# Kernel tuning notes

Measured on AMD Instinct MI355X. Metric: run time of the kernel, lower is better.

Reference implementation:

```python
import jax, jax.numpy as jnp
import numpy as np

BS, QLEN, DIM, NHEADS, SEG = 2, 2048, 640, 8, 5
C = DIM // SEG * (SEG - 1)  # 512, channels kept after aggregator
AGG = DIM // SEG            # 128, aggregated channel slice


def setup_inputs() -> dict:
    key = jax.random.key(0)
    ks = jax.random.split(key, 12)
    s = 0.02
    return {
        "Q": jax.random.normal(ks[0], (BS, QLEN, DIM), jnp.float32),
        # Linear weights stored [in, out] so y = x @ W + b
        "W_Q": jax.random.normal(ks[1], (DIM, DIM), jnp.float32) * s,
        "b_Q": jnp.zeros((DIM,), jnp.float32),
        "W_K": jax.random.normal(ks[2], (DIM, DIM), jnp.float32) * s,
        "b_K": jnp.zeros((DIM,), jnp.float32),
        "W_V": jax.random.normal(ks[3], (DIM, DIM), jnp.float32) * s,
        "b_V": jnp.zeros((DIM,), jnp.float32),
        "W_pos": jax.random.uniform(ks[4], (QLEN, C), jnp.float32, -0.02, 0.02),
        "W_agg": jax.random.normal(ks[5], (AGG, AGG), jnp.float32) * s,
        "b_agg": jnp.zeros((AGG,), jnp.float32),
        "W_out": jax.random.normal(ks[6], (DIM, DIM), jnp.float32) * s,
        "b_out": jnp.zeros((DIM,), jnp.float32),
    }


def reference(Q, W_Q, b_Q, W_K, b_K, W_V, b_V, W_pos, W_agg, b_agg, W_out, b_out):
    bs, L, dim = Q.shape
    hd = C // NHEADS  # per-head dim after aggregation (64)
    # self-attention: K = V = Q
    q = Q @ W_Q + b_Q
    k = Q @ W_K + b_K
    v = Q @ W_V + b_V
    qkv = jnp.stack([q, k, v])  # [3, bs, L, dim]
    # Aggregator: keep first 4/5 channels per branch, aggregate last 1/5 across q/k/v
    x_main = qkv[..., :C]                                   # [3, bs, L, C]
    x_agg0 = jax.nn.gelu(qkv[..., C:].mean(0) @ W_agg + b_agg)  # [bs, L, AGG]
    # pos embedding add (dropout is identity at eval)
    q_s = (x_main[0] + W_pos).reshape(bs, L, NHEADS, hd).transpose(0, 2, 1, 3)  # [bs,H,L,hd]
    k_s = (x_main[1] + W_pos).reshape(bs, L, NHEADS, hd).transpose(0, 2, 3, 1)  # [bs,H,hd,L]
    v_s = (x_main[2] + W_pos).reshape(bs, L, NHEADS, hd).transpose(0, 2, 1, 3)  # [bs,H,L,hd]
    scale = (DIM // NHEADS) ** -0.5  # note: uses dim//n_heads (80), not post-agg head dim
    scores = jnp.einsum("bhqd,bhdk->bhqk", q_s, k_s) * scale  # [bs,H,L,L]
    attn = jax.nn.softmax(scores, axis=-1)
    out = jnp.einsum("bhqk,bhkd->bhqd", attn, v_s)             # [bs,H,L,hd]
    out = out.transpose(0, 2, 1, 3).reshape(bs, L, C)
    out = jnp.concatenate([out, x_agg0], axis=-1) @ W_out + b_out  # [bs,L,dim]
    return out, attn
```

## Files before the change

### kernel.cpp

```cpp
#include <hip/hip_runtime.h>
#include <cstdint>
#include <cstddef>

#define BSZ   2
#define QL    2048
#define DIMN  640
#define NH    8
#define CMAIN 512
#define AGGD  128
#define MROWS 4096
#define SCALE_QK 0.11180339887498948f
#define C2EXP (SCALE_QK * 1.4426950408889634f)

typedef __bf16 bf16;
typedef __bf16 bf16x8 __attribute__((ext_vector_type(8)));
typedef __bf16 bf16x4v __attribute__((ext_vector_type(4)));
typedef float  f32x4  __attribute__((ext_vector_type(4)));

typedef __attribute__((address_space(1))) const uint32_t GU32;
typedef __attribute__((address_space(3))) uint32_t LU32;
#define GLL(g, l) __builtin_amdgcn_global_load_lds((GU32*)(g), (LU32*)(l), 16, 0, 0)

#define EXP2F(x) __builtin_amdgcn_exp2f(x)
#define LOG2F(x) __builtin_amdgcn_logf(x)

static __device__ __forceinline__ f32x4 mfma16(bf16x8 a, bf16x8 b, f32x4 c) {
    return __builtin_amdgcn_mfma_f32_16x16x32_bf16(a, b, c, 0, 0, 0);
}

static __device__ __forceinline__ void waitbar() {
    asm volatile("s_waitcnt vmcnt(0)" ::: "memory");
    __builtin_amdgcn_s_barrier();
    asm volatile("" ::: "memory");
}

template<int ROWB>
static __device__ __forceinline__ bf16x8 ldsfragR(const bf16* base, int row, int kbyte) {
    return *(const bf16x8*)((const char*)base + row * ROWB + (kbyte ^ ((row & 7) << 4)));
}

template<int NCH, int ROWB>
static __device__ __forceinline__ void stage_rowsR(bf16* ldsbuf, const char* gbase,
                                                   int strideB, int tid) {
    const int w = tid >> 6, lane = tid & 63;
    #pragma unroll
    for (int i = 0; i < NCH / 256; ++i) {
        int c = i * 256 + w * 64 + lane;
        int r = c / (ROWB / 16);
        int kb = ((c % (ROWB / 16)) * 16) ^ ((r & 7) << 4);
        GLL(gbase + (size_t)r * strideB + kb,
            (char*)ldsbuf + (size_t)(i * 256 + w * 64) * 16);
    }
}

template<int MI>
static __device__ __forceinline__ void gemm_main(
    const bf16* __restrict__ A, const bf16* __restrict__ BT,
    int m0, int n0, bf16* lds, f32x4 acc[MI][4])
{
    const int tid = threadIdx.x;
    const int w = tid >> 6, lane = tid & 63;
    const int lr = lane & 15, lg = lane >> 4;
    const int wm = (w >> 1) * (MI * 16), wn = (w & 1) * 64;
    constexpr int ASZ = MI * 2048;
    constexpr int BUF = ASZ + 8192;

    stage_rowsR<MI * 256, 128>(lds,   (const char*)(A + (size_t)m0 * 640), 1280, tid);
    stage_rowsR<1024, 128>(lds + ASZ, (const char*)(BT + (size_t)n0 * 640), 1280, tid);
    int cur = 0;
    #pragma unroll 1
    for (int ch = 0; ch < 10; ++ch) {
        waitbar();
        if (ch < 9) {
            int kk = (ch + 1) * 64;
            bf16* nb = lds + (cur ^ 1) * BUF;
            stage_rowsR<MI * 256, 128>(nb,   (const char*)(A + (size_t)m0 * 640 + kk), 1280, tid);
            stage_rowsR<1024, 128>(nb + ASZ, (const char*)(BT + (size_t)n0 * 640 + kk), 1280, tid);
        }
        const bf16* cA = lds + cur * BUF;
        const bf16* cB = cA + ASZ;
        #pragma unroll
        for (int ks = 0; ks < 2; ++ks) {
            bf16x8 a[MI], b[4];
            #pragma unroll
            for (int i = 0; i < MI; ++i) a[i] = ldsfragR<128>(cA, wm + i * 16 + lr, ks * 64 + lg * 16);
            #pragma unroll
            for (int i = 0; i < 4; ++i)  b[i] = ldsfragR<128>(cB, wn + i * 16 + lr, ks * 64 + lg * 16);
            #pragma unroll
            for (int mi = 0; mi < MI; ++mi)
                #pragma unroll
                for (int ni = 0; ni < 4; ++ni)
                    acc[mi][ni] = mfma16(a[mi], b[ni], acc[mi][ni]);
        }
        cur ^= 1;
    }
}

__global__ void __launch_bounds__(256) k_split_q(const float* __restrict__ Q,
                                                 bf16* __restrict__ Qbf) {
    int i = blockIdx.x * 256 + threadIdx.x;
    float4 v = ((const float4*)Q)[i];
    bf16x4v hv;
    hv[0] = (bf16)v.x; hv[1] = (bf16)v.y; hv[2] = (bf16)v.z; hv[3] = (bf16)v.w;
    *(bf16x4v*)(Qbf + (size_t)i * 4) = hv;
}

__global__ void __launch_bounds__(256) k_prep_w(
    const float* __restrict__ WQ, const float* __restrict__ WK,
    const float* __restrict__ WV, const float* __restrict__ WO,
    bf16* __restrict__ BTqkv, bf16* __restrict__ BTout)
{
    __shared__ float tl[64][65];
    const int ty = blockIdx.x / 10, tx = blockIdx.x % 10;
    const int wsel = blockIdx.y;
    const float* W = (wsel == 0) ? WQ : (wsel == 1) ? WK : (wsel == 2) ? WV : WO;
    const int tid = threadIdx.x;
    const int rr = tid >> 4;
    const int cc = (tid & 15) * 4;
    #pragma unroll
    for (int i = 0; i < 4; ++i) {
        int k = tx * 64 + rr + i * 16;
        float4 v = *(const float4*)(W + (size_t)k * 640 + ty * 64 + cc);
        tl[cc + 0][rr + i * 16] = v.x;
        tl[cc + 1][rr + i * 16] = v.y;
        tl[cc + 2][rr + i * 16] = v.z;
        tl[cc + 3][rr + i * 16] = v.w;
    }
    __syncthreads();
    bf16* dst; int nbase;
    if (wsel < 3) { dst = BTqkv; nbase = wsel * 640 + ty * 64; }
    else          { dst = BTout; nbase = ty * 64; }
    const int nl0 = tid >> 4;
    const int kl = (tid & 15) * 4;
    #pragma unroll
    for (int i = 0; i < 4; ++i) {
        int nl = nl0 + i * 16;
        bf16x4v hv;
        #pragma unroll
        for (int j = 0; j < 4; ++j) hv[j] = (bf16)tl[nl][kl + j];
        *(bf16x4v*)(dst + (size_t)(nbase + nl) * 640 + tx * 64 + kl) = hv;
    }
}

__global__ void __launch_bounds__(256) k_gemm_qkv(
    const bf16* __restrict__ Qbf, const bf16* __restrict__ BT,
    const float* __restrict__ bQ, const float* __restrict__ bK, const float* __restrict__ bV,
    const float* __restrict__ Wpos,
    bf16* __restrict__ qsbuf, bf16* __restrict__ vsT, float* __restrict__ aggbuf)
{
    __shared__ __align__(16) bf16 lds[2 * (8192 + 8192)];
    const int m0 = blockIdx.x * 128, n0 = blockIdx.y * 128;
    f32x4 acc[4][4];
    {
        f32x4 z = {0.f, 0.f, 0.f, 0.f};
        #pragma unroll
        for (int mi = 0; mi < 4; ++mi)
            #pragma unroll
            for (int ni = 0; ni < 4; ++ni) acc[mi][ni] = z;
    }
    gemm_main<4>(Qbf, BT, m0, n0, lds, acc);

    const int tid = threadIdx.x, w = tid >> 6, lane = tid & 63;
    const int lr = lane & 15, lg = lane >> 4;
    const int wm = (w >> 1) * 64, wn = (w & 1) * 64;
    const int p = n0 / 640;
    const float* bias = (p == 0) ? bQ : (p == 1) ? bK : bV;

    #pragma unroll
    for (int mi = 0; mi < 4; ++mi)
        #pragma unroll
        for (int ni = 0; ni < 4; ++ni) {
            int n = n0 + wn + ni * 16 + lr;
            int c = n - p * 640;
            int rbase = m0 + wm + mi * 16 + lg * 4;
            float bval = bias[c];
            if (c < 512) {
                int hh = c >> 6, d = c & 63;
                #pragma unroll
                for (int r = 0; r < 4; ++r) {
                    int rg = rbase + r;
                    int bb = rg >> 11, l = rg & 2047;
                    float v = acc[mi][ni][r] + bval + Wpos[(size_t)l * 512 + c];
                    if (p < 2)
                        qsbuf[(((size_t)(p * 2 + bb) * 8 + hh) * 2048 + l) * 64 + d] = (bf16)v;
                    else
                        vsT[(((size_t)(bb * 8 + hh)) * 64 + d) * 2048 + l] = (bf16)v;
                }
            } else {
                int j = c - 512;
                #pragma unroll
                for (int r = 0; r < 4; ++r) {
                    int rg = rbase + r;
                    aggbuf[((size_t)p * MROWS + rg) * AGGD + j] = acc[mi][ni][r] + bval;
                }
            }
        }
}

__global__ void __launch_bounds__(256) k_agg(const float* __restrict__ aggbuf,
                                             const float* __restrict__ Wagg, const float* __restrict__ bagg,
                                             bf16* __restrict__ xcat)
{
    __shared__ float wl[128 * 128];
    __shared__ float xl[32 * 128];
    const int tid = threadIdx.x;
    const int r0 = blockIdx.x * 32;
    for (int i = tid; i < 128 * 128; i += 256) wl[i] = Wagg[i];
    for (int i = tid; i < 32 * 128; i += 256) {
        int row = i >> 7, j = i & 127;
        size_t rg = r0 + row;
        float s = aggbuf[rg * AGGD + j]
                + aggbuf[((size_t)MROWS + rg) * AGGD + j]
                + aggbuf[((size_t)2 * MROWS + rg) * AGGD + j];
        xl[i] = s * (1.0f / 3.0f);
    }
    __syncthreads();
    const int row = tid >> 3;
    const int jo0 = (tid & 7) * 16;
    float acc[16];
    #pragma unroll
    for (int jj = 0; jj < 16; ++jj) acc[jj] = 0.f;
    for (int j = 0; j < 128; ++j) {
        float xv = xl[row * 128 + j];
        const float* wr = &wl[j * 128 + jo0];
        #pragma unroll
        for (int jj = 0; jj < 16; ++jj) acc[jj] = fmaf(xv, wr[jj], acc[jj]);
    }
    size_t rg = r0 + row;
    #pragma unroll
    for (int jj = 0; jj < 16; ++jj) {
        float t = acc[jj] + bagg[jo0 + jj];
        float g = 0.5f * t * (1.0f + tanhf(0.7978845608028654f * (t + 0.044715f * t * t * t)));
        xcat[rg * 640 + 512 + jo0 + jj] = (bf16)g;
    }
}

__global__ void __launch_bounds__(256) k_attn(const bf16* __restrict__ qsbuf, const bf16* __restrict__ vsT,
                                              float* __restrict__ gattn,
                                              bf16* __restrict__ xcat)
{
    __shared__ __align__(16) bf16 smem[2][16384];
    __shared__ __align__(16) bf16 p_lds[4][16 * 128];

    const int bh = blockIdx.y;
    const int b = bh >> 3, h = bh & 7;
    const int q0 = blockIdx.x * 64;
    const int tid = threadIdx.x, w = tid >> 6, lane = tid & 63;
    const int lr = lane & 15, lg = lane >> 4;

    const bf16* qbase = qsbuf + (size_t)(b * 8 + h) * (2048 * 64);
    const bf16* kbase = qsbuf + (size_t)((2 + b) * 8 + h) * (2048 * 64);
    const bf16* vtb   = vsT + (size_t)(b * 8 + h) * (64 * 2048);

    bf16x8 aq[2];
    {
        const bf16* qp = qbase + (size_t)(q0 + w * 16 + lr) * 64 + lg * 8;
        aq[0] = *(const bf16x8*)(qp);
        aq[1] = *(const bf16x8*)(qp + 32);
    }

    float lsum = 0.f;
    stage_rowsR<1024, 128>(smem[0], (const char*)kbase, 128, tid);
    int cur = 0;
    #pragma unroll 1
    for (int kt = 0; kt < 16; ++kt) {
        waitbar();
        if (kt < 15)
            stage_rowsR<1024, 128>(smem[cur ^ 1], (const char*)kbase + (size_t)(kt + 1) * 16384, 128, tid);
        __builtin_amdgcn_sched_barrier(0);
        const bf16* kb = smem[cur];
        f32x4 s[8];
        {
            f32x4 z = {0.f, 0.f, 0.f, 0.f};
            #pragma unroll
            for (int ni = 0; ni < 8; ++ni) s[ni] = z;
        }
        #pragma unroll
        for (int ks = 0; ks < 2; ++ks)
            #pragma unroll
            for (int ni = 0; ni < 8; ++ni)
                s[ni] = mfma16(ldsfragR<128>(kb, ni * 16 + lr, ks * 64 + lg * 16), aq[ks], s[ni]);
        #pragma unroll
        for (int ni = 0; ni < 8; ++ni)
            #pragma unroll
            for (int r = 0; r < 4; ++r)
                lsum += EXP2F(s[ni][r] * C2EXP);
        cur ^= 1;
    }
    lsum += __shfl_xor(lsum, 16);
    lsum += __shfl_xor(lsum, 32);
    const float l2i = -LOG2F(lsum);

    f32x4 o[4];
    {
        f32x4 z = {0.f, 0.f, 0.f, 0.f};
        #pragma unroll
        for (int ni = 0; ni < 4; ++ni) o[ni] = z;
    }
    float* attnrow = gattn + (size_t)bh * 2048 * 2048 + (size_t)(q0 + w * 16 + lr) * 2048;

    stage_rowsR<1024, 128>(smem[0],        (const char*)kbase, 128, tid);
    stage_rowsR<1024, 256>(smem[0] + 8192, (const char*)vtb, 4096, tid);
    cur = 0;
    #pragma unroll 1
    for (int kt = 0; kt < 16; ++kt) {
        if (kt == 0) asm volatile("s_waitcnt vmcnt(0)" ::: "memory");
        else         asm volatile("s_waitcnt vmcnt(8)" ::: "memory");
        __builtin_amdgcn_s_barrier();
        asm volatile("" ::: "memory");
        if (kt < 15) {
            stage_rowsR<1024, 128>(smem[cur ^ 1],        (const char*)kbase + (size_t)(kt + 1) * 16384, 128, tid);
            stage_rowsR<1024, 256>(smem[cur ^ 1] + 8192, (const char*)vtb + (size_t)(kt + 1) * 256, 4096, tid);
        }
        __builtin_amdgcn_sched_barrier(0);
        const bf16* kb = smem[cur];
        const bf16* vb = smem[cur] + 8192;
        f32x4 s[8];
        {
            f32x4 z = {0.f, 0.f, 0.f, 0.f};
            #pragma unroll
            for (int ni = 0; ni < 8; ++ni) s[ni] = z;
        }
        #pragma unroll
        for (int ks = 0; ks < 2; ++ks)
            #pragma unroll
            for (int ni = 0; ni < 8; ++ni)
                s[ni] = mfma16(ldsfragR<128>(kb, ni * 16 + lr, ks * 64 + lg * 16), aq[ks], s[ni]);
        bf16* pl = &p_lds[w][0];
        float* arow = attnrow + kt * 128;
        #pragma unroll
        for (int ni = 0; ni < 8; ++ni) {
            f32x4 p;
            #pragma unroll
            for (int r = 0; r < 4; ++r) p[r] = EXP2F(fmaf(s[ni][r], C2EXP, l2i));
            *(f32x4*)(arow + ni * 16 + lg * 4) = p;
            bf16x4v pb;
            #pragma unroll
            for (int r = 0; r < 4; ++r) pb[r] = (bf16)p[r];
            *(bf16x4v*)((char*)pl + lr * 256 + ((ni * 32 + lg * 8) ^ ((lr & 7) << 4))) = pb;
        }
        #pragma unroll
        for (int ks = 0; ks < 4; ++ks) {
            bf16x8 pa = ldsfragR<256>(pl, lr, ks * 64 + lg * 16);
            #pragma unroll
            for (int ni = 0; ni < 4; ++ni)
                o[ni] = mfma16(pa, ldsfragR<256>(vb, ni * 16 + lr, ks * 64 + lg * 16), o[ni]);
        }
        cur ^= 1;
    }

    #pragma unroll
    for (int ni = 0; ni < 4; ++ni) {
        #pragma unroll
        for (int r = 0; r < 4; ++r) {
            int qr = q0 + w * 16 + lg * 4 + r;
            size_t rg = (size_t)b * 2048 + qr;
            int c = h * 64 + ni * 16 + lr;
            xcat[rg * 640 + c] = (bf16)o[ni][r];
        }
    }
}

__global__ void __launch_bounds__(256) k_gemm_out(
    const bf16* __restrict__ X, const bf16* __restrict__ BT,
    const float* __restrict__ bout, float* __restrict__ out0)
{
    __shared__ __align__(16) bf16 lds[2 * (4096 + 8192)];
    const int m0 = blockIdx.x * 64, n0 = blockIdx.y * 128;
    f32x4 acc[2][4];
    {
        f32x4 z = {0.f, 0.f, 0.f, 0.f};
        #pragma unroll
        for (int mi = 0; mi < 2; ++mi)
            #pragma unroll
            for (int ni = 0; ni < 4; ++ni) acc[mi][ni] = z;
    }
    gemm_main<2>(X, BT, m0, n0, lds, acc);

    const int tid = threadIdx.x, w = tid >> 6, lane = tid & 63;
    const int lr = lane & 15, lg = lane >> 4;
    const int wm = (w >> 1) * 32, wn = (w & 1) * 64;
    #pragma unroll
    for (int mi = 0; mi < 2; ++mi)
        #pragma unroll
        for (int ni = 0; ni < 4; ++ni) {
            int n = n0 + wn + ni * 16 + lr;
            float bv = bout[n];
            #pragma unroll
            for (int r = 0; r < 4; ++r) {
                int rg = m0 + wm + mi * 16 + lg * 4 + r;
                out0[(size_t)rg * 640 + n] = acc[mi][ni][r] + bv;
            }
        }
}

extern "C" void kernel_launch(void* const* d_in, const int* in_sizes, int n_in,
                              void* d_out, int out_size, void* d_ws, size_t ws_size,
                              hipStream_t stream)
{
    (void)in_sizes; (void)n_in; (void)out_size; (void)ws_size;
    const float* Q    = (const float*)d_in[0];
    const float* WQ   = (const float*)d_in[1];
    const float* bQ   = (const float*)d_in[2];
    const float* WK   = (const float*)d_in[3];
    const float* bK   = (const float*)d_in[4];
    const float* WV   = (const float*)d_in[5];
    const float* bV   = (const float*)d_in[6];
    const float* Wpos = (const float*)d_in[7];
    const float* Wagg = (const float*)d_in[8];
    const float* bagg = (const float*)d_in[9];
    const float* WO   = (const float*)d_in[10];
    const float* bout = (const float*)d_in[11];

    float* out0  = (float*)d_out;
    float* gattn = out0 + (size_t)MROWS * DIMN;

    char* ws = (char*)d_ws;
    bf16* Qbf    = (bf16*)(ws);                 ws += (size_t)MROWS * DIMN * 2;
    bf16* BTqkv  = (bf16*)(ws);                 ws += (size_t)1920 * 640 * 2;
    bf16* BTout  = (bf16*)(ws);                 ws += (size_t)640 * 640 * 2;
    bf16* qsbuf  = (bf16*)(ws);                 ws += (size_t)4 * 8 * 2048 * 64 * 2;
    bf16* vsT    = (bf16*)(ws);                 ws += (size_t)16 * 64 * 2048 * 2;
    float* aggbuf= (float*)(ws);                ws += (size_t)3 * MROWS * AGGD * 4;
    bf16* xcat   = (bf16*)(ws);                 ws += (size_t)MROWS * DIMN * 2;

    k_split_q<<<dim3(2560), dim3(256), 0, stream>>>(Q, Qbf);
    k_prep_w<<<dim3(100, 4), dim3(256), 0, stream>>>(WQ, WK, WV, WO, BTqkv, BTout);
    k_gemm_qkv<<<dim3(32, 15), dim3(256), 0, stream>>>(Qbf, BTqkv,
                                                       bQ, bK, bV, Wpos, qsbuf, vsT, aggbuf);
    k_agg<<<dim3(128), dim3(256), 0, stream>>>(aggbuf, Wagg, bagg, xcat);
    k_attn<<<dim3(32, 16), dim3(256), 0, stream>>>(qsbuf, vsT, gattn, xcat);
    k_gemm_out<<<dim3(64, 5), dim3(256), 0, stream>>>(xcat, BTout, bout, out0);
}
```

Baseline: 157.9 us.

## Shrink attention blocks to two waves with 64-key tiles, swizzled grid, fused prep

The attention kernel moves from 256-thread blocks over 64 query rows to 128-thread blocks over 32 query rows. Its second pass now walks 64-key tiles instead of 128-key tiles, with smaller LDS buffers, and a flat grid that is swizzled across heads. The aim is more resident blocks per CU and better spread of the memory-bound attention-probability writes. The Q conversion and weight-transpose kernels are merged into one launch to save launch overhead. The cost is twice the barrier and staging iterations per key sweep, and the K tiles in the first pass are re-read by more blocks.

```diff
diff --git a/kernel.cpp b/kernel.cpp
--- a/kernel.cpp
+++ b/kernel.cpp
@@ -39,17 +39,18 @@
     return *(const bf16x8*)((const char*)base + row * ROWB + (kbyte ^ ((row & 7) << 4)));
 }
 
-template<int NCH, int ROWB>
+template<int NCH, int ROWB, int NT>
 static __device__ __forceinline__ void stage_rowsR(bf16* ldsbuf, const char* gbase,
                                                    int strideB, int tid) {
-    const int w = tid >> 6, lane = tid & 63;
-    #pragma unroll
-    for (int i = 0; i < NCH / 256; ++i) {
-        int c = i * 256 + w * 64 + lane;
+    const int lane = tid & 63;
+    const int wbase = tid - lane;
+    #pragma unroll
+    for (int i = 0; i < NCH / NT; ++i) {
+        int c = i * NT + tid;
         int r = c / (ROWB / 16);
         int kb = ((c % (ROWB / 16)) * 16) ^ ((r & 7) << 4);
         GLL(gbase + (size_t)r * strideB + kb,
-            (char*)ldsbuf + (size_t)(i * 256 + w * 64) * 16);
+            (char*)ldsbuf + (size_t)(i * NT + wbase) * 16);
     }
 }
 
@@ -65,8 +66,8 @@
     constexpr int ASZ = MI * 2048;
     constexpr int BUF = ASZ + 8192;
 
-    stage_rowsR<MI * 256, 128>(lds,   (const char*)(A + (size_t)m0 * 640), 1280, tid);
-    stage_rowsR<1024, 128>(lds + ASZ, (const char*)(BT + (size_t)n0 * 640), 1280, tid);
+    stage_rowsR<MI * 256, 128, 256>(lds,   (const char*)(A + (size_t)m0 * 640), 1280, tid);
+    stage_rowsR<1024, 128, 256>(lds + ASZ, (const char*)(BT + (size_t)n0 * 640), 1280, tid);
     int cur = 0;
     #pragma unroll 1
     for (int ch = 0; ch < 10; ++ch) {
@@ -74,8 +75,8 @@
         if (ch < 9) {
             int kk = (ch + 1) * 64;
             bf16* nb = lds + (cur ^ 1) * BUF;
-            stage_rowsR<MI * 256, 128>(nb,   (const char*)(A + (size_t)m0 * 640 + kk), 1280, tid);
-            stage_rowsR<1024, 128>(nb + ASZ, (const char*)(BT + (size_t)n0 * 640 + kk), 1280, tid);
+            stage_rowsR<MI * 256, 128, 256>(nb,   (const char*)(A + (size_t)m0 * 640 + kk), 1280, tid);
+            stage_rowsR<1024, 128, 256>(nb + ASZ, (const char*)(BT + (size_t)n0 * 640 + kk), 1280, tid);
         }
         const bf16* cA = lds + cur * BUF;
         const bf16* cB = cA + ASZ;
@@ -96,25 +97,27 @@
     }
 }
 
-__global__ void __launch_bounds__(256) k_split_q(const float* __restrict__ Q,
-                                                 bf16* __restrict__ Qbf) {
-    int i = blockIdx.x * 256 + threadIdx.x;
-    float4 v = ((const float4*)Q)[i];
-    bf16x4v hv;
-    hv[0] = (bf16)v.x; hv[1] = (bf16)v.y; hv[2] = (bf16)v.z; hv[3] = (bf16)v.w;
-    *(bf16x4v*)(Qbf + (size_t)i * 4) = hv;
-}
-
-__global__ void __launch_bounds__(256) k_prep_w(
-    const float* __restrict__ WQ, const float* __restrict__ WK,
-    const float* __restrict__ WV, const float* __restrict__ WO,
-    bf16* __restrict__ BTqkv, bf16* __restrict__ BTout)
+__global__ void __launch_bounds__(256) k_prep(
+    const float* __restrict__ Q, const float* __restrict__ WQ,
+    const float* __restrict__ WK, const float* __restrict__ WV,
+    const float* __restrict__ WO,
+    bf16* __restrict__ Qbf, bf16* __restrict__ BTqkv, bf16* __restrict__ BTout)
 {
     __shared__ float tl[64][65];
-    const int ty = blockIdx.x / 10, tx = blockIdx.x % 10;
-    const int wsel = blockIdx.y;
+    const int tid = threadIdx.x;
+    if (blockIdx.x < 2560) {
+        int i = blockIdx.x * 256 + tid;
+        float4 v = ((const float4*)Q)[i];
+        bf16x4v hv;
+        hv[0] = (bf16)v.x; hv[1] = (bf16)v.y; hv[2] = (bf16)v.z; hv[3] = (bf16)v.w;
+        *(bf16x4v*)(Qbf + (size_t)i * 4) = hv;
+        return;
+    }
+    const int f = blockIdx.x - 2560;
+    const int wsel = f / 100;
+    const int rem = f - wsel * 100;
+    const int ty = rem / 10, tx = rem - (rem / 10) * 10;
     const float* W = (wsel == 0) ? WQ : (wsel == 1) ? WK : (wsel == 2) ? WV : WO;
-    const int tid = threadIdx.x;
     const int rr = tid >> 4;
     const int cc = (tid & 15) * 4;
     #pragma unroll
@@ -235,16 +238,18 @@
     }
 }
 
-__global__ void __launch_bounds__(256) k_attn(const bf16* __restrict__ qsbuf, const bf16* __restrict__ vsT,
+__global__ void __launch_bounds__(128) k_attn(const bf16* __restrict__ qsbuf, const bf16* __restrict__ vsT,
                                               float* __restrict__ gattn,
                                               bf16* __restrict__ xcat)
 {
-    __shared__ __align__(16) bf16 smem[2][16384];
-    __shared__ __align__(16) bf16 p_lds[4][16 * 128];
-
-    const int bh = blockIdx.y;
+    __shared__ __align__(16) bf16 smem[2][8192];
+    __shared__ __align__(16) bf16 p_lds[2][1024];
+
+    const int flat = blockIdx.x;
+    const int swz = (flat & 7) * 128 + (flat >> 3);
+    const int bh = swz >> 6;
+    const int q0 = (swz & 63) * 32;
     const int b = bh >> 3, h = bh & 7;
-    const int q0 = blockIdx.x * 64;
     const int tid = threadIdx.x, w = tid >> 6, lane = tid & 63;
     const int lr = lane & 15, lg = lane >> 4;
 
@@ -260,13 +265,13 @@
     }
 
     float lsum = 0.f;
-    stage_rowsR<1024, 128>(smem[0], (const char*)kbase, 128, tid);
+    stage_rowsR<1024, 128, 128>(smem[0], (const char*)kbase, 128, tid);
     int cur = 0;
     #pragma unroll 1
     for (int kt = 0; kt < 16; ++kt) {
         waitbar();
         if (kt < 15)
-            stage_rowsR<1024, 128>(smem[cur ^ 1], (const char*)kbase + (size_t)(kt + 1) * 16384, 128, tid);
+            stage_rowsR<1024, 128, 128>(smem[cur ^ 1], (const char*)kbase + (size_t)(kt + 1) * 16384, 128, tid);
         __builtin_amdgcn_sched_barrier(0);
         const bf16* kb = smem[cur];
         f32x4 s[8];
@@ -299,37 +304,37 @@
     }
     float* attnrow = gattn + (size_t)bh * 2048 * 2048 + (size_t)(q0 + w * 16 + lr) * 2048;
 
-    stage_rowsR<1024, 128>(smem[0],        (const char*)kbase, 128, tid);
-    stage_rowsR<1024, 256>(smem[0] + 8192, (const char*)vtb, 4096, tid);
+    stage_rowsR<512, 128, 128>(smem[0],        (const char*)kbase, 128, tid);
+    stage_rowsR<512, 128, 128>(smem[0] + 4096, (const char*)vtb, 4096, tid);
     cur = 0;
     #pragma unroll 1
-    for (int kt = 0; kt < 16; ++kt) {
+    for (int kt = 0; kt < 32; ++kt) {
         if (kt == 0) asm volatile("s_waitcnt vmcnt(0)" ::: "memory");
-        else         asm volatile("s_waitcnt vmcnt(8)" ::: "memory");
+        else         asm volatile("s_waitcnt vmcnt(4)" ::: "memory");
         __builtin_amdgcn_s_barrier();
         asm volatile("" ::: "memory");
-        if (kt < 15) {
-            stage_rowsR<1024, 128>(smem[cur ^ 1],        (const char*)kbase + (size_t)(kt + 1) * 16384, 128, tid);
-            stage_rowsR<1024, 256>(smem[cur ^ 1] + 8192, (const char*)vtb + (size_t)(kt + 1) * 256, 4096, tid);
+        if (kt < 31) {
+            stage_rowsR<512, 128, 128>(smem[cur ^ 1],        (const char*)kbase + (size_t)(kt + 1) * 8192, 128, tid);
+            stage_rowsR<512, 128, 128>(smem[cur ^ 1] + 4096, (const char*)vtb + (size_t)(kt + 1) * 128, 4096, tid);
         }
         __builtin_amdgcn_sched_barrier(0);
         const bf16* kb = smem[cur];
-        const bf16* vb = smem[cur] + 8192;
-        f32x4 s[8];
+        const bf16* vb = smem[cur] + 4096;
+        f32x4 s[4];
         {
             f32x4 z = {0.f, 0.f, 0.f, 0.f};
             #pragma unroll
-            for (int ni = 0; ni < 8; ++ni) s[ni] = z;
+            for (int ni = 0; ni < 4; ++ni) s[ni] = z;
         }
         #pragma unroll
         for (int ks = 0; ks < 2; ++ks)
             #pragma unroll
-            for (int ni = 0; ni < 8; ++ni)
+            for (int ni = 0; ni < 4; ++ni)
                 s[ni] = mfma16(ldsfragR<128>(kb, ni * 16 + lr, ks * 64 + lg * 16), aq[ks], s[ni]);
         bf16* pl = &p_lds[w][0];
-        float* arow = attnrow + kt * 128;
-        #pragma unroll
-        for (int ni = 0; ni < 8; ++ni) {
+        float* arow = attnrow + kt * 64;
+        #pragma unroll
+        for (int ni = 0; ni < 4; ++ni) {
             f32x4 p;
             #pragma unroll
             for (int r = 0; r < 4; ++r) p[r] = EXP2F(fmaf(s[ni][r], C2EXP, l2i));
@@ -337,14 +342,14 @@
             bf16x4v pb;
             #pragma unroll
             for (int r = 0; r < 4; ++r) pb[r] = (bf16)p[r];
-            *(bf16x4v*)((char*)pl + lr * 256 + ((ni * 32 + lg * 8) ^ ((lr & 7) << 4))) = pb;
-        }
-        #pragma unroll
-        for (int ks = 0; ks < 4; ++ks) {
-            bf16x8 pa = ldsfragR<256>(pl, lr, ks * 64 + lg * 16);
+            *(bf16x4v*)((char*)pl + lr * 128 + ((ni * 32 + lg * 8) ^ ((lr & 7) << 4))) = pb;
+        }
+        #pragma unroll
+        for (int ks = 0; ks < 2; ++ks) {
+            bf16x8 pa = ldsfragR<128>(pl, lr, ks * 64 + lg * 16);
             #pragma unroll
             for (int ni = 0; ni < 4; ++ni)
-                o[ni] = mfma16(pa, ldsfragR<256>(vb, ni * 16 + lr, ks * 64 + lg * 16), o[ni]);
+                o[ni] = mfma16(pa, ldsfragR<128>(vb, ni * 16 + lr, ks * 64 + lg * 16), o[ni]);
         }
         cur ^= 1;
     }
@@ -424,11 +429,10 @@
     float* aggbuf= (float*)(ws);                ws += (size_t)3 * MROWS * AGGD * 4;
     bf16* xcat   = (bf16*)(ws);                 ws += (size_t)MROWS * DIMN * 2;
 
-    k_split_q<<<dim3(2560), dim3(256), 0, stream>>>(Q, Qbf);
-    k_prep_w<<<dim3(100, 4), dim3(256), 0, stream>>>(WQ, WK, WV, WO, BTqkv, BTout);
+    k_prep<<<dim3(2960), dim3(256), 0, stream>>>(Q, WQ, WK, WV, WO, Qbf, BTqkv, BTout);
     k_gemm_qkv<<<dim3(32, 15), dim3(256), 0, stream>>>(Qbf, BTqkv,
                                                        bQ, bK, bV, Wpos, qsbuf, vsT, aggbuf);
     k_agg<<<dim3(128), dim3(256), 0, stream>>>(aggbuf, Wagg, bagg, xcat);
-    k_attn<<<dim3(32, 16), dim3(256), 0, stream>>>(qsbuf, vsT, gattn, xcat);
+    k_attn<<<dim3(1024), dim3(128), 0, stream>>>(qsbuf, vsT, gattn, xcat);
     k_gemm_out<<<dim3(64, 5), dim3(256), 0, stream>>>(xcat, BTout, bout, out0);
 }
```

Result: slower. 164.4 us (+4.1%).
